# Performance work log

Measured on AMD Instinct MI355X. Metric: run time of the kernel, lower is better.

Reference implementation:

```python
import jax, jax.numpy as jnp
import numpy as np

H, V, L = 1024, 50257, 512

def setup_inputs() -> dict:
    key = jax.random.key(0)
    ks = jax.random.split(key, 14)
    s = 0.02
    return {
        "input": jax.random.randint(ks[0], (1,), 0, V),
        "hidden": jax.random.normal(ks[1], (1, 1, H), jnp.float32),
        "encoder_outputs": jax.random.normal(ks[2], (L, H), jnp.float32),
        "emb": jax.random.normal(ks[3], (V, H), jnp.float32) * s,
        "attn_w": jax.random.normal(ks[4], (L, 2 * H), jnp.float32) * s,
        "attn_b": jnp.zeros((L,), jnp.float32),
        "comb_w": jax.random.normal(ks[5], (H, 2 * H), jnp.float32) * s,
        "comb_b": jnp.zeros((H,), jnp.float32),
        "w_ih": jax.random.normal(ks[6], (3 * H, H), jnp.float32) * s,
        "w_hh": jax.random.normal(ks[7], (3 * H, H), jnp.float32) * s,
        "b_ih": jnp.zeros((3 * H,), jnp.float32),
        "b_hh": jnp.zeros((3 * H,), jnp.float32),
        "out_w": jax.random.normal(ks[8], (V, H), jnp.float32) * s,
        "out_b": jnp.zeros((V,), jnp.float32),
    }

def reference(input, hidden, encoder_outputs, emb, attn_w, attn_b,
              comb_w, comb_b, w_ih, w_hh, b_ih, b_hh, out_w, out_b):
    # embedding lookup (dropout is identity in eval mode)
    e = emb[input]                       # (1, H)
    h0 = hidden[0]                       # (1, H)
    # attention over encoder outputs
    scores = jnp.concatenate([e, h0], axis=1) @ attn_w.T + attn_b   # (1, L)
    attn_weights = jax.nn.softmax(scores, axis=1)                    # (1, L)
    attn_applied = attn_weights @ encoder_outputs                    # (1, H)
    # combine + relu
    x = jnp.concatenate([e, attn_applied], axis=1) @ comb_w.T + comb_b
    x = jax.nn.relu(x)                   # (1, H)
    # single GRU step (PyTorch gate layout: r, z, n)
    gi = x @ w_ih.T + b_ih               # (1, 3H)
    gh = h0 @ w_hh.T + b_hh              # (1, 3H)
    i_r, i_z, i_n = jnp.split(gi, 3, axis=1)
    h_r, h_z, h_n = jnp.split(gh, 3, axis=1)
    r = jax.nn.sigmoid(i_r + h_r)
    z = jax.nn.sigmoid(i_z + h_z)
    n = jnp.tanh(i_n + r * h_n)
    h_new = (1.0 - z) * n + z * h0       # (1, H)
    # output projection + log_softmax
    logits = h_new @ out_w.T + out_b     # (1, V)
    out = jax.nn.log_softmax(logits, axis=1)
    return out, h_new[None], attn_weights
```

## Files before the change

### kernel.cpp

```cpp
#include <hip/hip_runtime.h>

#define H 1024
#define L 512
#define V 50257
#define LOGIT_BLOCKS 2048

__device__ __forceinline__ float wave_reduce_sum(float v) {
    #pragma unroll
    for (int o = 32; o > 0; o >>= 1) v += __shfl_xor(v, o, 64);
    return v;
}

__global__ void k_scores(const float* __restrict__ emb, const int* __restrict__ input,
                         const float* __restrict__ hidden, const float* __restrict__ attn_w,
                         const float* __restrict__ attn_b, float* __restrict__ scores) {
    __shared__ float lds[4];
    int l = blockIdx.x, t = threadIdx.x;
    size_t erow = (size_t)input[0] * H;
    const float4* w = (const float4*)(attn_w + (size_t)l * 2 * H);
    float4 a  = w[t];
    float4 b  = w[256 + t];
    float4 ev = ((const float4*)(emb + erow))[t];
    float4 hv = ((const float4*)hidden)[t];
    float acc = a.x*ev.x + a.y*ev.y + a.z*ev.z + a.w*ev.w
              + b.x*hv.x + b.y*hv.y + b.z*hv.z + b.w*hv.w;
    acc = wave_reduce_sum(acc);
    int wid = t >> 6, lane = t & 63;
    if (lane == 0) lds[wid] = acc;
    __syncthreads();
    if (t == 0) scores[l] = lds[0] + lds[1] + lds[2] + lds[3] + attn_b[l];
}

__global__ void k_attn(const float* __restrict__ scores, const float* __restrict__ enc,
                       float* __restrict__ attn_out, float* __restrict__ attn_applied) {
    __shared__ float w[512];
    __shared__ float red[4];
    __shared__ float acc_lds[256];
    __shared__ float sM, sS;
    int t = threadIdx.x, lane = t & 63, wid = t >> 6;
    float s0 = scores[t], s1 = scores[t + 256];
    float m = fmaxf(s0, s1);
    #pragma unroll
    for (int o = 32; o > 0; o >>= 1) m = fmaxf(m, __shfl_xor(m, o, 64));
    if (lane == 0) red[wid] = m;
    __syncthreads();
    if (t == 0) sM = fmaxf(fmaxf(red[0], red[1]), fmaxf(red[2], red[3]));
    __syncthreads();
    float M = sM;
    float e0 = expf(s0 - M), e1 = expf(s1 - M);
    float s = e0 + e1;
    s = wave_reduce_sum(s);
    if (lane == 0) red[wid] = s;
    __syncthreads();
    if (t == 0) sS = red[0] + red[1] + red[2] + red[3];
    __syncthreads();
    float inv = 1.f / sS;
    w[t] = e0 * inv; w[t + 256] = e1 * inv;
    __syncthreads();
    if (blockIdx.x == 0) { attn_out[t] = w[t]; attn_out[t + 256] = w[t + 256]; }
    int col = blockIdx.x * 16 + (t & 15);
    int rc  = t >> 4;
    float acc = 0.f;
    #pragma unroll 8
    for (int l = rc; l < 512; l += 16)
        acc += w[l] * enc[(size_t)l * H + col];
    acc_lds[t] = acc;
    __syncthreads();
    #pragma unroll
    for (int st = 128; st >= 16; st >>= 1) {
        if (t < st) acc_lds[t] += acc_lds[t + st];
        __syncthreads();
    }
    if (t < 16) attn_applied[blockIdx.x * 16 + t] = acc_lds[t];
}

__global__ void k_combine(const float* __restrict__ emb, const int* __restrict__ input,
                          const float* __restrict__ attn_applied, const float* __restrict__ comb_w,
                          const float* __restrict__ comb_b, float* __restrict__ x) {
    __shared__ float lds[4];
    int h = blockIdx.x, t = threadIdx.x;
    size_t erow = (size_t)input[0] * H;
    const float4* w = (const float4*)(comb_w + (size_t)h * 2 * H);
    float4 a  = w[t];
    float4 b  = w[256 + t];
    float4 ev = ((const float4*)(emb + erow))[t];
    float4 av = ((const float4*)attn_applied)[t];
    float acc = a.x*ev.x + a.y*ev.y + a.z*ev.z + a.w*ev.w
              + b.x*av.x + b.y*av.y + b.z*av.z + b.w*av.w;
    acc = wave_reduce_sum(acc);
    int wid = t >> 6, lane = t & 63;
    if (lane == 0) lds[wid] = acc;
    __syncthreads();
    if (t == 0) x[h] = fmaxf(lds[0] + lds[1] + lds[2] + lds[3] + comb_b[h], 0.f);
}

__global__ void k_gru_fused(const float* __restrict__ w_ih, const float* __restrict__ w_hh,
                            const float* __restrict__ b_ih, const float* __restrict__ b_hh,
                            const float* __restrict__ x, const float* __restrict__ hidden,
                            float* __restrict__ hnew) {
    __shared__ float lds[4][6];
    int h = blockIdx.x, t = threadIdx.x, lane = t & 63, wid = t >> 6;
    float4 xv = ((const float4*)x)[t];
    float4 hv = ((const float4*)hidden)[t];
    const float* rows[6] = {
        w_ih + (size_t)h * H, w_ih + (size_t)(H + h) * H, w_ih + (size_t)(2 * H + h) * H,
        w_hh + (size_t)h * H, w_hh + (size_t)(H + h) * H, w_hh + (size_t)(2 * H + h) * H };
    float acc[6];
    #pragma unroll
    for (int k = 0; k < 6; ++k) {
        float4 wv = ((const float4*)rows[k])[t];
        float4 v  = (k < 3) ? xv : hv;
        acc[k] = wv.x*v.x + wv.y*v.y + wv.z*v.z + wv.w*v.w;
        acc[k] = wave_reduce_sum(acc[k]);
    }
    if (lane == 0) {
        #pragma unroll
        for (int k = 0; k < 6; ++k) lds[wid][k] = acc[k];
    }
    __syncthreads();
    if (t == 0) {
        float g[6];
        #pragma unroll
        for (int k = 0; k < 6; ++k) g[k] = lds[0][k] + lds[1][k] + lds[2][k] + lds[3][k];
        float ir = g[0] + b_ih[h],         hr = g[3] + b_hh[h];
        float iz = g[1] + b_ih[H + h],     hz = g[4] + b_hh[H + h];
        float in_ = g[2] + b_ih[2 * H + h], hn = g[5] + b_hh[2 * H + h];
        float r = 1.f / (1.f + expf(-(ir + hr)));
        float z = 1.f / (1.f + expf(-(iz + hz)));
        float n = tanhf(in_ + r * hn);
        hnew[h] = (1.f - z) * n + z * hidden[h];
    }
}

__global__ void k_logits_lse(const float* __restrict__ out_w, const float* __restrict__ out_b,
                             const float* __restrict__ hvec, float* __restrict__ logits,
                             float* __restrict__ mpart, float* __restrict__ spart) {
    __shared__ float lm[4], ls[4];
    int lane = threadIdx.x & 63, wid = threadIdx.x >> 6;
    int gwave = blockIdx.x * 4 + wid;
    const int nwaves = LOGIT_BLOCKS * 4;
    float4 h4[4];
    #pragma unroll
    for (int j = 0; j < 4; ++j) h4[j] = ((const float4*)hvec)[j * 64 + lane];
    float m = -INFINITY, s = 0.f;
    for (int r = gwave; r < V; r += nwaves) {
        const float4* row = (const float4*)(out_w + (size_t)r * H);
        float acc = 0.f;
        #pragma unroll
        for (int j = 0; j < 4; ++j) {
            float4 a = row[j * 64 + lane];
            acc += a.x*h4[j].x + a.y*h4[j].y + a.z*h4[j].z + a.w*h4[j].w;
        }
        acc = wave_reduce_sum(acc);
        float logit = acc + out_b[r];
        if (lane == 0) logits[r] = logit;
        if (logit > m) { s = s * expf(m - logit) + 1.f; m = logit; }
        else           { s += expf(logit - m); }
    }
    if (lane == 0) { lm[wid] = m; ls[wid] = s; }
    __syncthreads();
    if (threadIdx.x == 0) {
        float M = fmaxf(fmaxf(lm[0], lm[1]), fmaxf(lm[2], lm[3]));
        float S = 0.f;
        if (M > -INFINITY) {
            #pragma unroll
            for (int i = 0; i < 4; ++i) S += ls[i] * expf(lm[i] - M);
        }
        mpart[blockIdx.x] = M; spart[blockIdx.x] = S;
    }
}

__global__ void k_finalize(const float* __restrict__ mpart, const float* __restrict__ spart,
                           float* __restrict__ out) {
    __shared__ float lm[4], ls[4];
    __shared__ float sLogZ;
    int t = threadIdx.x, lane = t & 63, wid = t >> 6;
    float m = -INFINITY, s = 0.f;
    for (int i = t; i < LOGIT_BLOCKS; i += 256) {
        float m2 = mpart[i], s2 = spart[i];
        float mm = fmaxf(m, m2);
        if (mm > -INFINITY) s = s * expf(m - mm) + s2 * expf(m2 - mm);
        m = mm;
    }
    #pragma unroll
    for (int o = 32; o > 0; o >>= 1) {
        float m2 = __shfl_xor(m, o, 64), s2 = __shfl_xor(s, o, 64);
        float mm = fmaxf(m, m2);
        if (mm > -INFINITY) s = s * expf(m - mm) + s2 * expf(m2 - mm);
        m = mm;
    }
    if (lane == 0) { lm[wid] = m; ls[wid] = s; }
    __syncthreads();
    if (t == 0) {
        float M = fmaxf(fmaxf(lm[0], lm[1]), fmaxf(lm[2], lm[3]));
        float S = 0.f;
        #pragma unroll
        for (int i = 0; i < 4; ++i) S += ls[i] * expf(lm[i] - M);
        sLogZ = M + logf(S);
    }
    __syncthreads();
    int v = blockIdx.x * 256 + t;
    if (v < V) out[v] -= sLogZ;
}

extern "C" void kernel_launch(void* const* d_in, const int* in_sizes, int n_in,
                              void* d_out, int out_size, void* d_ws, size_t ws_size,
                              hipStream_t stream) {
    const int*   input  = (const int*)  d_in[0];
    const float* hidden = (const float*)d_in[1];
    const float* enc    = (const float*)d_in[2];
    const float* emb    = (const float*)d_in[3];
    const float* attn_w = (const float*)d_in[4];
    const float* attn_b = (const float*)d_in[5];
    const float* comb_w = (const float*)d_in[6];
    const float* comb_b = (const float*)d_in[7];
    const float* w_ih   = (const float*)d_in[8];
    const float* w_hh   = (const float*)d_in[9];
    const float* b_ih   = (const float*)d_in[10];
    const float* b_hh   = (const float*)d_in[11];
    const float* out_w  = (const float*)d_in[12];
    const float* out_b  = (const float*)d_in[13];

    float* out   = (float*)d_out;
    float* hnew  = out + V;
    float* attnw = out + V + H;

    float* ws           = (float*)d_ws;
    float* scores       = ws;
    float* attn_applied = ws + 512;
    float* xbuf         = ws + 1536;
    float* mpart        = ws + 2560;
    float* spart        = ws + 4608;

    k_scores     <<<512, 256, 0, stream>>>(emb, input, hidden, attn_w, attn_b, scores);
    k_attn       <<<64, 256, 0, stream>>>(scores, enc, attnw, attn_applied);
    k_combine    <<<1024, 256, 0, stream>>>(emb, input, attn_applied, comb_w, comb_b, xbuf);
    k_gru_fused  <<<1024, 256, 0, stream>>>(w_ih, w_hh, b_ih, b_hh, xbuf, hidden, hnew);
    k_logits_lse <<<LOGIT_BLOCKS, 256, 0, stream>>>(out_w, out_b, hnew, out, mpart, spart);
    k_finalize   <<<(V + 255) / 256, 256, 0, stream>>>(mpart, spart, out);
}
```

Measured before the change: 61.44 us.

## Hoist hidden- and embedding-dependent matvecs into the first kernel

Moves the w_hh·h GRU matvec and the embedding half of the combine matvec out of the dependent chain and into a widened first kernel alongside the attention scores. Later kernels then read only the halves of the weights that depend on attention or combine output, which shortens the critical-path work after attention. The cost is a larger first launch (4608 blocks) with branchy task dispatch, plus extra workspace buffers for the partial results.

```diff
diff --git a/kernel.cpp b/kernel.cpp
--- a/kernel.cpp
+++ b/kernel.cpp
@@ -5,30 +5,45 @@
 #define V 50257
 #define LOGIT_BLOCKS 2048
 
+__device__ __forceinline__ float dot4(float4 a, float4 b) {
+    return a.x*b.x + a.y*b.y + a.z*b.z + a.w*b.w;
+}
+
 __device__ __forceinline__ float wave_reduce_sum(float v) {
     #pragma unroll
     for (int o = 32; o > 0; o >>= 1) v += __shfl_xor(v, o, 64);
     return v;
 }
 
-__global__ void k_scores(const float* __restrict__ emb, const int* __restrict__ input,
-                         const float* __restrict__ hidden, const float* __restrict__ attn_w,
-                         const float* __restrict__ attn_b, float* __restrict__ scores) {
-    __shared__ float lds[4];
-    int l = blockIdx.x, t = threadIdx.x;
+__global__ void k_pre(const float* __restrict__ emb, const int* __restrict__ input,
+                      const float* __restrict__ hidden, const float* __restrict__ attn_w,
+                      const float* __restrict__ attn_b, const float* __restrict__ w_hh,
+                      const float* __restrict__ b_hh, const float* __restrict__ comb_w,
+                      float* __restrict__ scores, float* __restrict__ gh, float* __restrict__ ce) {
+    __shared__ float red[4];
+    int task = blockIdx.x, t = threadIdx.x, lane = t & 63, wid = t >> 6;
     size_t erow = (size_t)input[0] * H;
-    const float4* w = (const float4*)(attn_w + (size_t)l * 2 * H);
-    float4 a  = w[t];
-    float4 b  = w[256 + t];
-    float4 ev = ((const float4*)(emb + erow))[t];
-    float4 hv = ((const float4*)hidden)[t];
-    float acc = a.x*ev.x + a.y*ev.y + a.z*ev.z + a.w*ev.w
-              + b.x*hv.x + b.y*hv.y + b.z*hv.z + b.w*hv.w;
+    float acc;
+    if (task < 512) {
+        const float4* w = (const float4*)(attn_w + (size_t)task * (2 * H));
+        acc = dot4(w[t], ((const float4*)(emb + erow))[t])
+            + dot4(w[256 + t], ((const float4*)hidden)[t]);
+    } else if (task < 3584) {
+        int j = task - 512;
+        acc = dot4(((const float4*)(w_hh + (size_t)j * H))[t], ((const float4*)hidden)[t]);
+    } else {
+        int h = task - 3584;
+        acc = dot4(((const float4*)(comb_w + (size_t)h * (2 * H)))[t], ((const float4*)(emb + erow))[t]);
+    }
     acc = wave_reduce_sum(acc);
-    int wid = t >> 6, lane = t & 63;
-    if (lane == 0) lds[wid] = acc;
-    __syncthreads();
-    if (t == 0) scores[l] = lds[0] + lds[1] + lds[2] + lds[3] + attn_b[l];
+    if (lane == 0) red[wid] = acc;
+    __syncthreads();
+    if (t == 0) {
+        float s = red[0] + red[1] + red[2] + red[3];
+        if (task < 512)       scores[task] = s + attn_b[task];
+        else if (task < 3584) { int j = task - 512; gh[j] = s + b_hh[j]; }
+        else                  ce[task - 3584] = s;
+    }
 }
 
 __global__ void k_attn(const float* __restrict__ scores, const float* __restrict__ enc,
@@ -48,8 +63,7 @@
     __syncthreads();
     float M = sM;
     float e0 = expf(s0 - M), e1 = expf(s1 - M);
-    float s = e0 + e1;
-    s = wave_reduce_sum(s);
+    float s = wave_reduce_sum(e0 + e1);
     if (lane == 0) red[wid] = s;
     __syncthreads();
     if (t == 0) sS = red[0] + red[1] + red[2] + red[3];
@@ -62,8 +76,7 @@
     int rc  = t >> 4;
     float acc = 0.f;
     #pragma unroll 8
-    for (int l = rc; l < 512; l += 16)
-        acc += w[l] * enc[(size_t)l * H + col];
+    for (int l = rc; l < 512; l += 16) acc += w[l] * enc[(size_t)l * H + col];
     acc_lds[t] = acc;
     __syncthreads();
     #pragma unroll
@@ -74,60 +87,43 @@
     if (t < 16) attn_applied[blockIdx.x * 16 + t] = acc_lds[t];
 }
 
-__global__ void k_combine(const float* __restrict__ emb, const int* __restrict__ input,
-                          const float* __restrict__ attn_applied, const float* __restrict__ comb_w,
-                          const float* __restrict__ comb_b, float* __restrict__ x) {
-    __shared__ float lds[4];
-    int h = blockIdx.x, t = threadIdx.x;
-    size_t erow = (size_t)input[0] * H;
-    const float4* w = (const float4*)(comb_w + (size_t)h * 2 * H);
-    float4 a  = w[t];
-    float4 b  = w[256 + t];
-    float4 ev = ((const float4*)(emb + erow))[t];
-    float4 av = ((const float4*)attn_applied)[t];
-    float acc = a.x*ev.x + a.y*ev.y + a.z*ev.z + a.w*ev.w
-              + b.x*av.x + b.y*av.y + b.z*av.z + b.w*av.w;
+__global__ void k_combine2(const float* __restrict__ ce, const float* __restrict__ attn_applied,
+                           const float* __restrict__ comb_w, const float* __restrict__ comb_b,
+                           float* __restrict__ x) {
+    __shared__ float red[4];
+    int h = blockIdx.x, t = threadIdx.x, lane = t & 63, wid = t >> 6;
+    float acc = dot4(((const float4*)(comb_w + (size_t)h * (2 * H) + H))[t],
+                     ((const float4*)attn_applied)[t]);
     acc = wave_reduce_sum(acc);
-    int wid = t >> 6, lane = t & 63;
-    if (lane == 0) lds[wid] = acc;
-    __syncthreads();
-    if (t == 0) x[h] = fmaxf(lds[0] + lds[1] + lds[2] + lds[3] + comb_b[h], 0.f);
-}
-
-__global__ void k_gru_fused(const float* __restrict__ w_ih, const float* __restrict__ w_hh,
-                            const float* __restrict__ b_ih, const float* __restrict__ b_hh,
-                            const float* __restrict__ x, const float* __restrict__ hidden,
-                            float* __restrict__ hnew) {
-    __shared__ float lds[4][6];
+    if (lane == 0) red[wid] = acc;
+    __syncthreads();
+    if (t == 0)
+        x[h] = fmaxf(ce[h] + red[0] + red[1] + red[2] + red[3] + comb_b[h], 0.f);
+}
+
+__global__ void k_gru2(const float* __restrict__ w_ih, const float* __restrict__ b_ih,
+                       const float* __restrict__ gh, const float* __restrict__ x,
+                       const float* __restrict__ hidden, float* __restrict__ hnew) {
+    __shared__ float red[12];
     int h = blockIdx.x, t = threadIdx.x, lane = t & 63, wid = t >> 6;
     float4 xv = ((const float4*)x)[t];
-    float4 hv = ((const float4*)hidden)[t];
-    const float* rows[6] = {
-        w_ih + (size_t)h * H, w_ih + (size_t)(H + h) * H, w_ih + (size_t)(2 * H + h) * H,
-        w_hh + (size_t)h * H, w_hh + (size_t)(H + h) * H, w_hh + (size_t)(2 * H + h) * H };
-    float acc[6];
-    #pragma unroll
-    for (int k = 0; k < 6; ++k) {
-        float4 wv = ((const float4*)rows[k])[t];
-        float4 v  = (k < 3) ? xv : hv;
-        acc[k] = wv.x*v.x + wv.y*v.y + wv.z*v.z + wv.w*v.w;
-        acc[k] = wave_reduce_sum(acc[k]);
-    }
-    if (lane == 0) {
+    float a0 = dot4(((const float4*)(w_ih + (size_t)h * H))[t], xv);
+    float a1 = dot4(((const float4*)(w_ih + (size_t)(H + h) * H))[t], xv);
+    float a2 = dot4(((const float4*)(w_ih + (size_t)(2 * H + h) * H))[t], xv);
+    a0 = wave_reduce_sum(a0);
+    a1 = wave_reduce_sum(a1);
+    a2 = wave_reduce_sum(a2);
+    if (lane == 0) { red[wid * 3] = a0; red[wid * 3 + 1] = a1; red[wid * 3 + 2] = a2; }
+    __syncthreads();
+    if (t == 0) {
+        float g0 = 0.f, g1 = 0.f, g2 = 0.f;
         #pragma unroll
-        for (int k = 0; k < 6; ++k) lds[wid][k] = acc[k];
-    }
-    __syncthreads();
-    if (t == 0) {
-        float g[6];
-        #pragma unroll
-        for (int k = 0; k < 6; ++k) g[k] = lds[0][k] + lds[1][k] + lds[2][k] + lds[3][k];
-        float ir = g[0] + b_ih[h],         hr = g[3] + b_hh[h];
-        float iz = g[1] + b_ih[H + h],     hz = g[4] + b_hh[H + h];
-        float in_ = g[2] + b_ih[2 * H + h], hn = g[5] + b_hh[2 * H + h];
-        float r = 1.f / (1.f + expf(-(ir + hr)));
-        float z = 1.f / (1.f + expf(-(iz + hz)));
-        float n = tanhf(in_ + r * hn);
+        for (int w2 = 0; w2 < 4; ++w2) {
+            g0 += red[w2 * 3]; g1 += red[w2 * 3 + 1]; g2 += red[w2 * 3 + 2];
+        }
+        float r = 1.f / (1.f + expf(-(g0 + b_ih[h] + gh[h])));
+        float z = 1.f / (1.f + expf(-(g1 + b_ih[H + h] + gh[H + h])));
+        float n = tanhf(g2 + b_ih[2 * H + h] + r * gh[2 * H + h]);
         hnew[h] = (1.f - z) * n + z * hidden[h];
     }
 }
@@ -147,10 +143,7 @@
         const float4* row = (const float4*)(out_w + (size_t)r * H);
         float acc = 0.f;
         #pragma unroll
-        for (int j = 0; j < 4; ++j) {
-            float4 a = row[j * 64 + lane];
-            acc += a.x*h4[j].x + a.y*h4[j].y + a.z*h4[j].z + a.w*h4[j].w;
-        }
+        for (int j = 0; j < 4; ++j) acc += dot4(row[j * 64 + lane], h4[j]);
         acc = wave_reduce_sum(acc);
         float logit = acc + out_b[r];
         if (lane == 0) logits[r] = logit;
@@ -227,15 +220,18 @@
 
     float* ws           = (float*)d_ws;
     float* scores       = ws;
-    float* attn_applied = ws + 512;
-    float* xbuf         = ws + 1536;
-    float* mpart        = ws + 2560;
-    float* spart        = ws + 4608;
-
-    k_scores     <<<512, 256, 0, stream>>>(emb, input, hidden, attn_w, attn_b, scores);
+    float* gh           = ws + 512;
+    float* ce           = ws + 3584;
+    float* attn_applied = ws + 4608;
+    float* xbuf         = ws + 5632;
+    float* mpart        = ws + 6656;
+    float* spart        = ws + 8704;
+
+    k_pre        <<<4608, 256, 0, stream>>>(emb, input, hidden, attn_w, attn_b,
+                                            w_hh, b_hh, comb_w, scores, gh, ce);
     k_attn       <<<64, 256, 0, stream>>>(scores, enc, attnw, attn_applied);
-    k_combine    <<<1024, 256, 0, stream>>>(emb, input, attn_applied, comb_w, comb_b, xbuf);
-    k_gru_fused  <<<1024, 256, 0, stream>>>(w_ih, w_hh, b_ih, b_hh, xbuf, hidden, hnew);
+    k_combine2   <<<1024, 256, 0, stream>>>(ce, attn_applied, comb_w, comb_b, xbuf);
+    k_gru2       <<<1024, 256, 0, stream>>>(w_ih, b_ih, gh, xbuf, hidden, hnew);
     k_logits_lse <<<LOGIT_BLOCKS, 256, 0, stream>>>(out_w, out_b, hnew, out, mpart, spart);
     k_finalize   <<<(V + 255) / 256, 256, 0, stream>>>(mpart, spart, out);
 }
```

Result: faster. 59.83 us (-2.6%).
